# Optimization experiments

Hardware: AMD Instinct MI355X
Metric: run time of the kernel (lower is better)

Reference implementation:

```python
import jax, jax.numpy as jnp
import numpy as np

B, F, C, NS, P, N = 256, 2048, 16384, 65536, 8, 32
T, W_BU, W_H, P_MARGIN, N_MARGIN = 1.0, 1.0, 10.0, 0.1, 0.1


def setup_inputs() -> dict:
    key = jax.random.key(0)
    ks = jax.random.split(key, 8)
    inputs = jax.random.normal(ks[0], (B, F), jnp.float32)
    targets = jax.random.randint(ks[1], (B,), 0, C)
    # batch global indices: unique (original .item() assumes a single match)
    indexs = jax.random.permutation(ks[2], NS)[:B].astype(jnp.int64) if False else jax.random.permutation(ks[2], jnp.arange(NS))[:B]
    # positive candidates drawn from in-batch indices so they are found in `indexs`
    pos_sel = jax.random.randint(ks[3], (B, P), 0, B)
    ppairs = indexs[pos_sel]
    # negative candidates: arbitrary global indices (mostly not in batch)
    npairs = jax.random.randint(ks[4], (B, N), 0, NS)
    all_label_to_clusterid = jax.random.randint(ks[5], (NS,), 0, C)
    V = jax.random.normal(ks[6], (C, F), jnp.float32)
    V = V / jnp.linalg.norm(V, axis=1, keepdims=True)  # bank rows are L2-normalized by the update rule
    return {"inputs": inputs, "targets": targets, "ppairs": ppairs, "npairs": npairs,
            "indexs": indexs, "all_label_to_clusterid": all_label_to_clusterid, "V": V, "epoch": 1}


def _forward(inputs, targets, ppairs, npairs, indexs, all_label_to_clusterid, V, epoch):
    # Exclusive branch: logits against the memory bank (V treated as constant)
    outputs = (inputs @ V.T) * T  # [B, C]
    logp = jax.nn.log_softmax(outputs, axis=1)
    bu_loss = -jnp.mean(jnp.take_along_axis(logp, targets[:, None], axis=1))

    # ms_loss (use_prior=True, use_table=True)
    ni = inputs / jnp.linalg.norm(inputs, axis=1, keepdims=True)
    sims = ni @ ni.T          # [B, B]
    tsims = ni @ V.T          # [B, C]

    # positives found in the batch: (ppair == indexs).nonzero()
    mp = ppairs[:, :, None] == indexs[None, None, :]        # [B, P, B]
    found_p = jnp.any(mp, axis=2)
    idx_p = jnp.argmax(mp, axis=2)
    psim_b = jnp.take_along_axis(sims, idx_p, axis=1)       # [B, P]
    mask_pb = found_p & (ppairs >= 0)
    # table positive: tsims[i, target] appended if nonzero
    tp = jnp.take_along_axis(tsims, targets[:, None], axis=1)  # [B, 1]
    mask_tp = tp != 0
    psims = jnp.concatenate([psim_b, tp], axis=1)           # [B, P+1]
    pmask = jnp.concatenate([mask_pb, mask_tp], axis=1)

    # negatives found in the batch
    mn = npairs[:, :, None] == indexs[None, None, :]        # [B, N, B]
    found_n = jnp.any(mn, axis=2)
    idx_n = jnp.argmax(mn, axis=2)
    nsim_b = jnp.take_along_axis(sims, idx_n, axis=1)       # [B, N]
    mask_nb = found_n & (npairs >= 0)
    # table negative appended for EVERY npair (indent level in original): tsims[i, clusterid[npair]]
    ncid = all_label_to_clusterid[jnp.clip(npairs, 0, None)]
    tn = jnp.take_along_axis(tsims, ncid, axis=1)           # [B, N]
    mask_tn = (npairs >= 0) & (tn != 0)
    nsims = jnp.concatenate([nsim_b, tn], axis=1)           # [B, 2N]
    nmask = jnp.concatenate([mask_nb, mask_tn], axis=1)

    # thresholds: max(nsims) or -3 (+p_margin); min(psims) or 3 (-n_margin)
    p_thrd = jnp.where(jnp.any(nmask, 1), jnp.max(jnp.where(nmask, nsims, -jnp.inf), 1), -3.0) + P_MARGIN
    n_thrd = jnp.where(jnp.any(pmask, 1), jnp.min(jnp.where(pmask, psims, jnp.inf), 1), 3.0) - N_MARGIN

    hp = pmask & (psims < p_thrd[:, None])
    hn = nmask & (nsims > n_thrd[:, None]) & (nsims < 0.999999)

    hp_sum = jnp.sum(jnp.where(hp, jnp.exp(-2.0 * (psims - 0.5)), 0.0))
    hn_sum = jnp.sum(jnp.where(hn, jnp.exp(50.0 * (nsims - 0.5)), 0.0))
    hp_loss = jnp.where(jnp.any(hp), 0.5 * jnp.log1p(hp_sum), 0.0)
    hn_loss = jnp.where(jnp.any(hn), (1.0 / 50.0) * jnp.log1p(hn_sum), 0.0)
    # original builds hpsims/hnsims with torch.tensor(...), which DETACHES them
    h_loss = jax.lax.stop_gradient(hp_loss + hn_loss)

    loss = W_BU * bu_loss + W_H * h_loss
    return loss, outputs


def reference(inputs, targets, ppairs, npairs, indexs, all_label_to_clusterid, V, epoch):
    return _forward(inputs, targets, ppairs, npairs, indexs, all_label_to_clusterid, V, epoch)
```

## Files before the change

### kernel.cpp

```cpp
#include <hip/hip_runtime.h>
#include <hip/hip_bf16.h>
#include <math.h>

#define B_SZ 256
#define F_SZ 2048
#define C_SZ 16384
#define P_SZ 8
#define N_SZ 32

typedef __bf16 bf16x8 __attribute__((ext_vector_type(8)));
typedef float f32x4 __attribute__((ext_vector_type(4)));
typedef unsigned short us8 __attribute__((ext_vector_type(8)));

__device__ __forceinline__ unsigned short f2bf(float x) {
    union { float f; unsigned int u; } v; v.f = x;
    unsigned int r = v.u + 0x7FFFu + ((v.u >> 16) & 1u);
    return (unsigned short)(r >> 16);
}

__global__ __launch_bounds__(256) void prep_kernel(const float* __restrict__ inputs,
                                                   unsigned short* __restrict__ Abf,
                                                   float* __restrict__ norms) {
    const int row = blockIdx.x;
    const int tid = threadIdx.x;
    const float* rp = inputs + (size_t)row * F_SZ + tid * 8;
    float4 v0 = *(const float4*)(rp);
    float4 v1 = *(const float4*)(rp + 4);
    us8 o;
    o[0]=f2bf(v0.x); o[1]=f2bf(v0.y); o[2]=f2bf(v0.z); o[3]=f2bf(v0.w);
    o[4]=f2bf(v1.x); o[5]=f2bf(v1.y); o[6]=f2bf(v1.z); o[7]=f2bf(v1.w);
    *(us8*)(Abf + (size_t)row * F_SZ + tid * 8) = o;
    float ss = v0.x*v0.x + v0.y*v0.y + v0.z*v0.z + v0.w*v0.w
             + v1.x*v1.x + v1.y*v1.y + v1.z*v1.z + v1.w*v1.w;
    __shared__ float red[256];
    red[tid] = ss; __syncthreads();
    for (int s = 128; s > 0; s >>= 1) { if (tid < s) red[tid] += red[tid+s]; __syncthreads(); }
    if (tid == 0) norms[row] = sqrtf(red[0]);
}

#define BM 64
#define BN 128
#define BK 32
#define LDK 40

__global__ __launch_bounds__(256) void gemm_kernel(const unsigned short* __restrict__ Abf,
                                                   const float* __restrict__ V,
                                                   float* __restrict__ Cout) {
    __shared__ unsigned short As[BM * LDK];
    __shared__ unsigned short Bs[BN * LDK];
    const int tid = threadIdx.x;
    const int lane = tid & 63;
    const int wid = tid >> 6;
    const int wm = wid >> 1, wn = wid & 1;
    const int q = lane >> 4, l16 = lane & 15;
    const int bm0 = blockIdx.y * BM;
    const int bn0 = blockIdx.x * BN;

    f32x4 acc[2][4];
    #pragma unroll
    for (int i = 0; i < 2; i++)
        #pragma unroll
        for (int j = 0; j < 4; j++) acc[i][j] = (f32x4){0.f, 0.f, 0.f, 0.f};

    const int ar = tid >> 2, aseg = tid & 3;
    const unsigned short* Ag = Abf + (size_t)(bm0 + ar) * F_SZ + aseg * 8;
    unsigned short* Asd = &As[ar * LDK + aseg * 8];

    const int br = tid >> 1, bseg = tid & 1;
    const float* Bg = V + (size_t)(bn0 + br) * F_SZ + bseg * 16;
    unsigned short* Bsd = &Bs[br * LDK + bseg * 16];

    for (int k0 = 0; k0 < F_SZ; k0 += BK) {
        us8 av = *(const us8*)(Ag + k0);
        float4 b0 = *(const float4*)(Bg + k0);
        float4 b1 = *(const float4*)(Bg + k0 + 4);
        float4 b2 = *(const float4*)(Bg + k0 + 8);
        float4 b3 = *(const float4*)(Bg + k0 + 12);
        __syncthreads();
        *(us8*)Asd = av;
        us8 w0, w1;
        w0[0]=f2bf(b0.x); w0[1]=f2bf(b0.y); w0[2]=f2bf(b0.z); w0[3]=f2bf(b0.w);
        w0[4]=f2bf(b1.x); w0[5]=f2bf(b1.y); w0[6]=f2bf(b1.z); w0[7]=f2bf(b1.w);
        w1[0]=f2bf(b2.x); w1[1]=f2bf(b2.y); w1[2]=f2bf(b2.z); w1[3]=f2bf(b2.w);
        w1[4]=f2bf(b3.x); w1[5]=f2bf(b3.y); w1[6]=f2bf(b3.z); w1[7]=f2bf(b3.w);
        *(us8*)Bsd = w0;
        *(us8*)(Bsd + 8) = w1;
        __syncthreads();

        bf16x8 af[2], bfv[4];
        #pragma unroll
        for (int mi = 0; mi < 2; mi++)
            af[mi] = *(const bf16x8*)&As[(wm*32 + mi*16 + l16) * LDK + q*8];
        #pragma unroll
        for (int ni = 0; ni < 4; ni++)
            bfv[ni] = *(const bf16x8*)&Bs[(wn*64 + ni*16 + l16) * LDK + q*8];
        #pragma unroll
        for (int mi = 0; mi < 2; mi++)
            #pragma unroll
            for (int ni = 0; ni < 4; ni++)
                acc[mi][ni] = __builtin_amdgcn_mfma_f32_16x16x32_bf16(af[mi], bfv[ni], acc[mi][ni], 0, 0, 0);
    }

    #pragma unroll
    for (int mi = 0; mi < 2; mi++) {
        const int r0 = bm0 + wm*32 + mi*16 + q*4;
        #pragma unroll
        for (int ni = 0; ni < 4; ni++) {
            const int c0 = bn0 + wn*64 + ni*16 + l16;
            #pragma unroll
            for (int r = 0; r < 4; r++)
                Cout[(size_t)(r0 + r) * C_SZ + c0] = acc[mi][ni][r];
        }
    }
}

__global__ __launch_bounds__(256) void loss_rows_kernel(
    const float* __restrict__ inputs, const int* __restrict__ targets,
    const int* __restrict__ ppairs, const int* __restrict__ npairs,
    const int* __restrict__ indexs, const int* __restrict__ cluster,
    const float* __restrict__ outputs, const float* __restrict__ norms,
    float* __restrict__ bu_part, float* __restrict__ hp_part,
    float* __restrict__ hn_part, int* __restrict__ flag_part)
{
    const int i = blockIdx.x;
    const int tid = threadIdx.x;
    __shared__ int idxbuf[B_SZ];
    __shared__ int pj[P_SZ];
    __shared__ int nj[N_SZ];
    __shared__ float simp[P_SZ];
    __shared__ float simn[N_SZ];
    __shared__ float tnv[N_SZ];
    __shared__ float red[256];
    __shared__ float s_max, s_tp;

    idxbuf[tid] = indexs[tid];
    __syncthreads();

    const float* row = outputs + (size_t)i * C_SZ;
    const float ni_norm = norms[i];

    float m = -INFINITY;
    for (int c = tid; c < C_SZ; c += 256) m = fmaxf(m, row[c]);
    red[tid] = m; __syncthreads();
    for (int s = 128; s > 0; s >>= 1) { if (tid < s) red[tid] = fmaxf(red[tid], red[tid+s]); __syncthreads(); }
    if (tid == 0) s_max = red[0];
    __syncthreads();
    const float mx = s_max;
    float se = 0.f;
    for (int c = tid; c < C_SZ; c += 256) se += expf(row[c] - mx);
    red[tid] = se; __syncthreads();
    for (int s = 128; s > 0; s >>= 1) { if (tid < s) red[tid] += red[tid+s]; __syncthreads(); }

    if (tid < P_SZ) {
        int pp = ppairs[i * P_SZ + tid];
        int f = -1;
        if (pp >= 0) for (int j = 0; j < B_SZ; j++) if (idxbuf[j] == pp) { f = j; break; }
        pj[tid] = f;
    } else if (tid < P_SZ + N_SZ) {
        int t = tid - P_SZ;
        int np = npairs[i * N_SZ + t];
        int f = -1;
        if (np >= 0) for (int j = 0; j < B_SZ; j++) if (idxbuf[j] == np) { f = j; break; }
        nj[t] = f;
        int cid = cluster[np < 0 ? 0 : np];
        tnv[t] = row[cid] / ni_norm;
    }
    if (tid == P_SZ + N_SZ) s_tp = row[targets[i]] / ni_norm;
    __syncthreads();

    const int lane = tid & 63, wv = tid >> 6;
    for (int qq = wv; qq < P_SZ + N_SZ; qq += 4) {
        int j = (qq < P_SZ) ? pj[qq] : nj[qq - P_SZ];
        float s = 0.f;
        if (j >= 0) {
            const float* xi = inputs + (size_t)i * F_SZ;
            const float* xj = inputs + (size_t)j * F_SZ;
            float d = 0.f;
            for (int k = lane; k < F_SZ; k += 64) d += xi[k] * xj[k];
            for (int off = 32; off > 0; off >>= 1) d += __shfl_down(d, off);
            s = d / (ni_norm * norms[j]);
        }
        if (lane == 0) { if (qq < P_SZ) simp[qq] = s; else simn[qq - P_SZ] = s; }
    }
    __syncthreads();

    if (tid == 0) {
        float logZ = mx + logf(red[0]);
        bu_part[i] = -(row[targets[i]] - logZ);

        float psims[P_SZ + 1]; bool pmask[P_SZ + 1];
        for (int p = 0; p < P_SZ; p++) {
            int pp = ppairs[i * P_SZ + p];
            pmask[p] = (pj[p] >= 0) && (pp >= 0);
            psims[p] = simp[p];
        }
        psims[P_SZ] = s_tp; pmask[P_SZ] = (s_tp != 0.0f);

        float nsims[2 * N_SZ]; bool nmask[2 * N_SZ];
        for (int t = 0; t < N_SZ; t++) {
            int np = npairs[i * N_SZ + t];
            nmask[t] = (nj[t] >= 0) && (np >= 0);
            nsims[t] = simn[t];
            nsims[N_SZ + t] = tnv[t];
            nmask[N_SZ + t] = (np >= 0) && (tnv[t] != 0.0f);
        }
        bool anyp = false, anyn = false;
        float maxn = -INFINITY, minp = INFINITY;
        for (int t = 0; t < 2 * N_SZ; t++) if (nmask[t]) { anyn = true; maxn = fmaxf(maxn, nsims[t]); }
        for (int p = 0; p < P_SZ + 1; p++) if (pmask[p]) { anyp = true; minp = fminf(minp, psims[p]); }
        float p_thrd = (anyn ? maxn : -3.0f) + 0.1f;
        float n_thrd = (anyp ? minp : 3.0f) - 0.1f;
        float hps = 0.f, hns = 0.f; int fl = 0;
        for (int p = 0; p < P_SZ + 1; p++)
            if (pmask[p] && psims[p] < p_thrd) { fl |= 1; hps += expf(-2.0f * (psims[p] - 0.5f)); }
        for (int t = 0; t < 2 * N_SZ; t++)
            if (nmask[t] && nsims[t] > n_thrd && nsims[t] < 0.999999f) { fl |= 2; hns += expf(50.0f * (nsims[t] - 0.5f)); }
        hp_part[i] = hps; hn_part[i] = hns; flag_part[i] = fl;
    }
}

__global__ __launch_bounds__(256) void finalize_kernel(
    const float* __restrict__ bu_part, const float* __restrict__ hp_part,
    const float* __restrict__ hn_part, const int* __restrict__ flag_part,
    float* __restrict__ d_out)
{
    __shared__ float r1[256], r2[256], r3[256];
    __shared__ int rf[256];
    const int tid = threadIdx.x;
    r1[tid] = bu_part[tid]; r2[tid] = hp_part[tid]; r3[tid] = hn_part[tid]; rf[tid] = flag_part[tid];
    __syncthreads();
    for (int s = 128; s > 0; s >>= 1) {
        if (tid < s) { r1[tid] += r1[tid+s]; r2[tid] += r2[tid+s]; r3[tid] += r3[tid+s]; rf[tid] |= rf[tid+s]; }
        __syncthreads();
    }
    if (tid == 0) {
        float bu = r1[0] / (float)B_SZ;
        float hp_loss = (rf[0] & 1) ? 0.5f * log1pf(r2[0]) : 0.0f;
        float hn_loss = (rf[0] & 2) ? (1.0f / 50.0f) * log1pf(r3[0]) : 0.0f;
        d_out[0] = 1.0f * bu + 10.0f * (hp_loss + hn_loss);
    }
}

extern "C" void kernel_launch(void* const* d_in, const int* in_sizes, int n_in,
                              void* d_out, int out_size, void* d_ws, size_t ws_size,
                              hipStream_t stream) {
    const float* inputs  = (const float*)d_in[0];
    const int*   targets = (const int*)d_in[1];
    const int*   ppairs  = (const int*)d_in[2];
    const int*   npairs  = (const int*)d_in[3];
    const int*   indexs  = (const int*)d_in[4];
    const int*   cluster = (const int*)d_in[5];
    const float* V       = (const float*)d_in[6];
    float* out = (float*)d_out;

    char* ws = (char*)d_ws;
    unsigned short* Abf = (unsigned short*)ws;
    float* norms   = (float*)(ws + (size_t)B_SZ * F_SZ * 2);
    float* bu_part = norms + B_SZ;
    float* hp_part = bu_part + B_SZ;
    float* hn_part = hp_part + B_SZ;
    int*   flag_part = (int*)(hn_part + B_SZ);

    prep_kernel<<<B_SZ, 256, 0, stream>>>(inputs, Abf, norms);
    gemm_kernel<<<dim3(C_SZ / BN, B_SZ / BM), 256, 0, stream>>>(Abf, V, out + 1);
    loss_rows_kernel<<<B_SZ, 256, 0, stream>>>(inputs, targets, ppairs, npairs, indexs,
                                               cluster, out + 1, norms,
                                               bu_part, hp_part, hn_part, flag_part);
    finalize_kernel<<<1, 256, 0, stream>>>(bu_part, hp_part, hn_part, flag_part, out);
}
```

Baseline: 340.8 us.

## Double-buffer GEMM with async A loads, XOR-swizzled LDS, and online softmax

The GEMM now double-buffers LDS, issuing direct global-to-LDS loads for the bf16 A tile and register-prefetching the fp32 V tile for the next K step while MFMAs run on the current one. It also changes the tile shape to 128x64 with BK=64 and uses an XOR swizzle on the A tile to avoid bank conflicts. The loss kernel replaces its two-pass max-then-sum-exp over each logits row with a single-pass online softmax using fast __expf. The costs are more LDS per block and some loss of precision from the fast exp.

Result: faster. 316.9 us (-7.0%).

```diff
diff --git a/kernel.cpp b/kernel.cpp
--- a/kernel.cpp
+++ b/kernel.cpp
@@ -11,6 +11,9 @@
 typedef __bf16 bf16x8 __attribute__((ext_vector_type(8)));
 typedef float f32x4 __attribute__((ext_vector_type(4)));
 typedef unsigned short us8 __attribute__((ext_vector_type(8)));
+
+typedef __attribute__((address_space(3))) unsigned int lds_u32;
+typedef __attribute__((address_space(1))) const unsigned int glb_u32;
 
 __device__ __forceinline__ unsigned short f2bf(float x) {
     union { float f; unsigned int u; } v; v.f = x;
@@ -38,20 +41,21 @@
     if (tid == 0) norms[row] = sqrtf(red[0]);
 }
 
-#define BM 64
-#define BN 128
-#define BK 32
-#define LDK 40
+#define BM 128
+#define BN 64
+#define BK 64
+#define BPAD 72
+#define KITERS (F_SZ / BK)
 
 __global__ __launch_bounds__(256) void gemm_kernel(const unsigned short* __restrict__ Abf,
                                                    const float* __restrict__ V,
                                                    float* __restrict__ Cout) {
-    __shared__ unsigned short As[BM * LDK];
-    __shared__ unsigned short Bs[BN * LDK];
+    __shared__ unsigned short As[2][BM * BK];
+    __shared__ unsigned short Bs[2][BN * BPAD];
+
     const int tid = threadIdx.x;
     const int lane = tid & 63;
     const int wid = tid >> 6;
-    const int wm = wid >> 1, wn = wid & 1;
     const int q = lane >> 4, l16 = lane & 15;
     const int bm0 = blockIdx.y * BM;
     const int bn0 = blockIdx.x * BN;
@@ -62,53 +66,84 @@
         #pragma unroll
         for (int j = 0; j < 4; j++) acc[i][j] = (f32x4){0.f, 0.f, 0.f, 0.f};
 
-    const int ar = tid >> 2, aseg = tid & 3;
-    const unsigned short* Ag = Abf + (size_t)(bm0 + ar) * F_SZ + aseg * 8;
-    unsigned short* Asd = &As[ar * LDK + aseg * 8];
-
-    const int br = tid >> 1, bseg = tid & 1;
-    const float* Bg = V + (size_t)(bn0 + br) * F_SZ + bseg * 16;
-    unsigned short* Bsd = &Bs[br * LDK + bseg * 16];
-
-    for (int k0 = 0; k0 < F_SZ; k0 += BK) {
-        us8 av = *(const us8*)(Ag + k0);
-        float4 b0 = *(const float4*)(Bg + k0);
-        float4 b1 = *(const float4*)(Bg + k0 + 4);
-        float4 b2 = *(const float4*)(Bg + k0 + 8);
-        float4 b3 = *(const float4*)(Bg + k0 + 12);
-        __syncthreads();
-        *(us8*)Asd = av;
+    const int arow = tid >> 3;
+    const int cfetch = (tid & 7) ^ (arow & 7);
+    const unsigned short* AgBase = Abf + (size_t)(bm0 + arow) * F_SZ + cfetch * 8;
+
+    const int brow = tid >> 2, bseg = tid & 3;
+    const float* BgBase = V + (size_t)(bn0 + brow) * F_SZ + bseg * 16;
+    unsigned short* Bsd0 = &Bs[0][brow * BPAD + bseg * 16];
+    unsigned short* Bsd1 = &Bs[1][brow * BPAD + bseg * 16];
+
+    float4 b0, b1, b2, b3;
+
+    auto issueA = [&](int buf, int k0) {
+        #pragma unroll
+        for (int j = 0; j < 4; j++) {
+            __builtin_amdgcn_global_load_lds(
+                (glb_u32*)(AgBase + (size_t)j * 32 * F_SZ + k0),
+                (lds_u32*)&As[buf][(size_t)(j * 256 + wid * 64) * 8],
+                16, 0, 0);
+        }
+    };
+    auto loadB = [&](int k0) {
+        b0 = *(const float4*)(BgBase + k0);
+        b1 = *(const float4*)(BgBase + k0 + 4);
+        b2 = *(const float4*)(BgBase + k0 + 8);
+        b3 = *(const float4*)(BgBase + k0 + 12);
+    };
+    auto writeB = [&](unsigned short* dst) {
         us8 w0, w1;
         w0[0]=f2bf(b0.x); w0[1]=f2bf(b0.y); w0[2]=f2bf(b0.z); w0[3]=f2bf(b0.w);
         w0[4]=f2bf(b1.x); w0[5]=f2bf(b1.y); w0[6]=f2bf(b1.z); w0[7]=f2bf(b1.w);
         w1[0]=f2bf(b2.x); w1[1]=f2bf(b2.y); w1[2]=f2bf(b2.z); w1[3]=f2bf(b2.w);
         w1[4]=f2bf(b3.x); w1[5]=f2bf(b3.y); w1[6]=f2bf(b3.z); w1[7]=f2bf(b3.w);
-        *(us8*)Bsd = w0;
-        *(us8*)(Bsd + 8) = w1;
+        *(us8*)dst = w0;
+        *(us8*)(dst + 8) = w1;
+    };
+
+    issueA(0, 0);
+    loadB(0);
+    writeB(Bsd0);
+    __syncthreads();
+
+    for (int it = 0; it < KITERS; ++it) {
+        const int cur = it & 1;
+        const bool more = (it + 1) < KITERS;
+        if (more) {
+            issueA(cur ^ 1, (it + 1) * BK);
+            loadB((it + 1) * BK);
+        }
+        #pragma unroll
+        for (int ks = 0; ks < 2; ++ks) {
+            bf16x8 af[2], bfv[4];
+            #pragma unroll
+            for (int mi = 0; mi < 2; ++mi) {
+                const int row = wid * 32 + mi * 16 + l16;
+                const int kc = ks * 4 + q;
+                af[mi] = *(const bf16x8*)&As[cur][(size_t)(row * 8 + (kc ^ (row & 7))) * 8];
+            }
+            #pragma unroll
+            for (int ni = 0; ni < 4; ++ni)
+                bfv[ni] = *(const bf16x8*)&Bs[cur][(ni * 16 + l16) * BPAD + ks * 32 + q * 8];
+            #pragma unroll
+            for (int mi = 0; mi < 2; ++mi)
+                #pragma unroll
+                for (int ni = 0; ni < 4; ++ni)
+                    acc[mi][ni] = __builtin_amdgcn_mfma_f32_16x16x32_bf16(af[mi], bfv[ni], acc[mi][ni], 0, 0, 0);
+        }
+        if (more) writeB(cur ? Bsd0 : Bsd1);
         __syncthreads();
-
-        bf16x8 af[2], bfv[4];
+    }
+
+    #pragma unroll
+    for (int mi = 0; mi < 2; ++mi) {
+        const int r0 = bm0 + wid * 32 + mi * 16 + q * 4;
         #pragma unroll
-        for (int mi = 0; mi < 2; mi++)
-            af[mi] = *(const bf16x8*)&As[(wm*32 + mi*16 + l16) * LDK + q*8];
-        #pragma unroll
-        for (int ni = 0; ni < 4; ni++)
-            bfv[ni] = *(const bf16x8*)&Bs[(wn*64 + ni*16 + l16) * LDK + q*8];
-        #pragma unroll
-        for (int mi = 0; mi < 2; mi++)
+        for (int ni = 0; ni < 4; ++ni) {
+            const int c0 = bn0 + ni * 16 + l16;
             #pragma unroll
-            for (int ni = 0; ni < 4; ni++)
-                acc[mi][ni] = __builtin_amdgcn_mfma_f32_16x16x32_bf16(af[mi], bfv[ni], acc[mi][ni], 0, 0, 0);
-    }
-
-    #pragma unroll
-    for (int mi = 0; mi < 2; mi++) {
-        const int r0 = bm0 + wm*32 + mi*16 + q*4;
-        #pragma unroll
-        for (int ni = 0; ni < 4; ni++) {
-            const int c0 = bn0 + wn*64 + ni*16 + l16;
-            #pragma unroll
-            for (int r = 0; r < 4; r++)
+            for (int r = 0; r < 4; ++r)
                 Cout[(size_t)(r0 + r) * C_SZ + c0] = acc[mi][ni][r];
         }
     }
@@ -130,8 +165,8 @@
     __shared__ float simp[P_SZ];
     __shared__ float simn[N_SZ];
     __shared__ float tnv[N_SZ];
-    __shared__ float red[256];
-    __shared__ float s_max, s_tp;
+    __shared__ float red_m[256], red_s[256];
+    __shared__ float s_tp;
 
     idxbuf[tid] = indexs[tid];
     __syncthreads();
@@ -139,17 +174,24 @@
     const float* row = outputs + (size_t)i * C_SZ;
     const float ni_norm = norms[i];
 
-    float m = -INFINITY;
-    for (int c = tid; c < C_SZ; c += 256) m = fmaxf(m, row[c]);
-    red[tid] = m; __syncthreads();
-    for (int s = 128; s > 0; s >>= 1) { if (tid < s) red[tid] = fmaxf(red[tid], red[tid+s]); __syncthreads(); }
-    if (tid == 0) s_max = red[0];
-    __syncthreads();
-    const float mx = s_max;
-    float se = 0.f;
-    for (int c = tid; c < C_SZ; c += 256) se += expf(row[c] - mx);
-    red[tid] = se; __syncthreads();
-    for (int s = 128; s > 0; s >>= 1) { if (tid < s) red[tid] += red[tid+s]; __syncthreads(); }
+    float m = -INFINITY, se = 0.f;
+    for (int c = tid; c < C_SZ; c += 256) {
+        float v = row[c];
+        float nm = fmaxf(m, v);
+        se = se * __expf(m - nm) + __expf(v - nm);
+        m = nm;
+    }
+    red_m[tid] = m; red_s[tid] = se; __syncthreads();
+    for (int s = 128; s > 0; s >>= 1) {
+        if (tid < s) {
+            float m2 = red_m[tid + s], s2 = red_s[tid + s];
+            float m1 = red_m[tid],      s1 = red_s[tid];
+            float nm = fmaxf(m1, m2);
+            red_s[tid] = s1 * __expf(m1 - nm) + s2 * __expf(m2 - nm);
+            red_m[tid] = nm;
+        }
+        __syncthreads();
+    }
 
     if (tid < P_SZ) {
         int pp = ppairs[i * P_SZ + tid];
@@ -185,7 +227,7 @@
     __syncthreads();
 
     if (tid == 0) {
-        float logZ = mx + logf(red[0]);
+        float logZ = red_m[0] + logf(red_s[0]);
         bu_part[i] = -(row[targets[i]] - logZ);
 
         float psims[P_SZ + 1]; bool pmask[P_SZ + 1];
```
